# Optimization experiments

Measured on AMD Instinct MI355X. Metric: run time of the kernel, lower is better.

Reference implementation:

```python
import jax, jax.numpy as jnp
import numpy as np

B, SIZE_IN, SIZE_OUT = 64, 1024, 1024


def setup_inputs() -> dict:
    key = jax.random.key(0)
    ks = jax.random.split(key, 6)
    mu_in = jax.random.normal(ks[0], (B, SIZE_IN), jnp.float32)
    # PSD input covariance: low-rank + jitter (sigma_in is a covariance matrix)
    L = jax.random.normal(ks[1], (B, SIZE_IN, 16), jnp.float32)
    sigma_in = jnp.einsum('bik,bjk->bij', L, L) / 16.0 + 1e-3 * jnp.eye(SIZE_IN, dtype=jnp.float32)
    bound = (1.0 / SIZE_IN) ** 0.5
    w_mu = jax.random.uniform(ks[2], (SIZE_IN, SIZE_OUT), jnp.float32, -bound, bound)
    b_mu = jax.random.uniform(ks[3], (SIZE_OUT, 1), jnp.float32, -bound, bound)
    w_sigma = jax.random.uniform(ks[4], (SIZE_OUT, SIZE_IN), jnp.float32, -12.0, -2.0)
    b_sigma = jax.random.uniform(ks[5], (SIZE_OUT,), jnp.float32, -12.0, -2.0)
    return {"mu_in": mu_in, "sigma_in": sigma_in, "w_mu": w_mu,
            "w_sigma": w_sigma, "b_mu": b_mu, "b_sigma": b_sigma}


def reference(mu_in, sigma_in, w_mu, w_sigma, b_mu, b_sigma):
    Bsz, n = mu_in.shape            # n = size_in
    m = w_mu.shape[1]               # m = size_out
    # mean propagation: (B, m, 1)
    mu_out = jnp.einsum('io,bi->bo', w_mu, mu_in)[:, :, None] + b_mu
    # diagonal weight/bias variances (softplus + epsilon), kept as vectors
    W_Sig = jax.nn.softplus(w_sigma) + 1e-6   # (m, n) == diag of diag_embed(W_Sigma)[o]
    B_Sig = jax.nn.softplus(b_sigma) + 1e-6   # (m,)
    # mu_in^T diag(W_Sig[o]) mu_in  -> (B, m)
    quad = jnp.einsum('oi,bi->bo', W_Sig, mu_in * mu_in)
    # faithful replication of torch's .view-based "trace" term:
    # W_Sigma.view(m, n*n) @ sigma_in.view(n*n, B), then result.view(B, m).
    # diag_embed rows only hit flat indices i*(n+1), so gather those rows.
    sig_flat = sigma_in.reshape(n * n, Bsz)            # memory reinterpret, like torch .view
    diag_rows = sig_flat[jnp.arange(n) * (n + 1)]      # (n, B)
    trW = (W_Sig @ diag_rows).reshape(Bsz, m)          # memory reinterpret, like torch .view
    # w_mu^T sigma_in w_mu : (B, m, m) -- dominant GEMM
    muT_sig_mu = jnp.einsum('io,bij,jp->bop', w_mu, sigma_in, w_mu)
    diag_term = trW + quad + B_Sig[None, :]            # (B, m)
    Sigma_out = muT_sig_mu + diag_term[:, :, None] * jnp.eye(m, dtype=mu_in.dtype)
    # KL vs standard normal; slogdet of a positive diagonal matrix == sum(log(diag))
    w_kl = 0.5 * jnp.sum(jnp.sum(W_Sig, axis=1) + jnp.sum(w_mu * w_mu, axis=0)
                         - n - jnp.sum(jnp.log(W_Sig), axis=1))
    b_kl = 0.5 * (jnp.sum(B_Sig) + jnp.sum(b_mu * b_mu) - m - jnp.sum(jnp.log(B_Sig)))
    return (mu_out, Sigma_out, w_kl, b_kl)
```

## Files before the change

### kernel.cpp

```cpp
#include <hip/hip_runtime.h>
#include <hip/hip_bf16.h>


typedef short bf16x8 __attribute__((ext_vector_type(8)));
typedef float f32x4  __attribute__((ext_vector_type(4)));
typedef unsigned short u16x8 __attribute__((ext_vector_type(8)));

__device__ __forceinline__ unsigned short f2bf(float f) {
    union { float f; unsigned u; } a; a.f = f;
    unsigned u = a.u;
    u += 0x7fffu + ((u >> 16) & 1u);
    return (unsigned short)(u >> 16);
}

__device__ __forceinline__ float softplus_eps(float x) {
    return fmaxf(x, 0.f) + log1pf(expf(-fabsf(x))) + 1e-6f;
}

__device__ __forceinline__ void gload_lds16(const unsigned short* g, unsigned short* l) {
    __builtin_amdgcn_global_load_lds(
        (const __attribute__((address_space(1))) void*)g,
        (__attribute__((address_space(3))) void*)l, 16, 0, 0);
}


__global__ void k_zero(float* acc) {
    if (threadIdx.x < 16) acc[threadIdx.x] = 0.f;
}

__global__ void k_convert(const float* __restrict__ src, unsigned short* __restrict__ dst) {
    const size_t i = ((size_t)blockIdx.x * 256 + threadIdx.x) * 8;
    const float4 a = *(const float4*)(src + i);
    const float4 b = *(const float4*)(src + i + 4);
    u16x8 h;
    h[0] = f2bf(a.x); h[1] = f2bf(a.y); h[2] = f2bf(a.z); h[3] = f2bf(a.w);
    h[4] = f2bf(b.x); h[5] = f2bf(b.y); h[6] = f2bf(b.z); h[7] = f2bf(b.w);
    *(u16x8*)(dst + i) = h;
}

__global__ void k_transpose(const float* __restrict__ wmu, float* __restrict__ wT32,
                            unsigned short* __restrict__ wTb, float* __restrict__ acc) {
    __shared__ float tile[64][65];
    const int bx = blockIdx.x;
    const int by = blockIdx.y;
    const int t = threadIdx.x;
    const int r = t >> 4;
    const int c4 = (t & 15) * 4;
    float s = 0.f;
#pragma unroll
    for (int p = 0; p < 4; ++p) {
        const int row = r + p * 16;
        const float4 v = *(const float4*)(wmu + (size_t)(bx * 64 + row) * 1024 + by * 64 + c4);
        tile[row][c4 + 0] = v.x; tile[row][c4 + 1] = v.y;
        tile[row][c4 + 2] = v.z; tile[row][c4 + 3] = v.w;
        s += v.x * v.x + v.y * v.y + v.z * v.z + v.w * v.w;
    }
    __syncthreads();
#pragma unroll
    for (int p = 0; p < 4; ++p) {
        const int row = r + p * 16;
        float4 o;
        o.x = tile[c4 + 0][row]; o.y = tile[c4 + 1][row];
        o.z = tile[c4 + 2][row]; o.w = tile[c4 + 3][row];
        const size_t off = (size_t)(by * 64 + row) * 1024 + bx * 64 + c4;
        *(float4*)(wT32 + off) = o;
        ushort4 h; h.x = f2bf(o.x); h.y = f2bf(o.y); h.z = f2bf(o.z); h.w = f2bf(o.w);
        *(ushort4*)(wTb + off) = h;
    }
#pragma unroll
    for (int off = 32; off; off >>= 1) s += __shfl_down(s, off, 64);
    if ((t & 63) == 0) atomicAdd(acc + 1, s);
}

__global__ void k_wsig(const float* __restrict__ wsg, float* __restrict__ WSig,
                       float* __restrict__ acc) {
    const int idx = (blockIdx.x * 256 + threadIdx.x) * 4;
    const float4 x = *(const float4*)(wsg + idx);
    float4 w;
    w.x = softplus_eps(x.x); w.y = softplus_eps(x.y);
    w.z = softplus_eps(x.z); w.w = softplus_eps(x.w);
    *(float4*)(WSig + idx) = w;
    float sw = w.x + w.y + w.z + w.w;
    float sl = logf(w.x) + logf(w.y) + logf(w.z) + logf(w.w);
#pragma unroll
    for (int off = 32; off; off >>= 1) {
        sw += __shfl_down(sw, off, 64);
        sl += __shfl_down(sl, off, 64);
    }
    if ((threadIdx.x & 63) == 0) { atomicAdd(acc + 0, sw); atomicAdd(acc + 2, sl); }
}

__global__ void k_gather(const float* __restrict__ sig, float* __restrict__ dr) {
    const int tg = blockIdx.x * 256 + threadIdx.x;
    const int k = tg >> 6, q = tg & 63;
    dr[tg] = sig[(size_t)k * 65600 + q];
}

__global__ void k_small(const float* __restrict__ mu_in, const float* __restrict__ wT32,
                        const float* __restrict__ WSig, const float* __restrict__ dr,
                        const float* __restrict__ b_mu, const float* __restrict__ b_sig,
                        float* __restrict__ mu_out, float* __restrict__ dterm) {
    __shared__ float mu_s[1024];
    __shared__ float m2_s[1024];
    const int blk = blockIdx.x;
    const int b = blk >> 2;
    const int o0 = (blk & 3) * 256;
    const int t = threadIdx.x;
    const int o = o0 + t;
    for (int j = t; j < 1024; j += 256) {
        const float v = mu_in[b * 1024 + j];
        mu_s[j] = v; m2_s[j] = v * v;
    }
    __syncthreads();
    const int rowTr = b * 16 + (o >> 6);
    const int qq = o & 63;
    const float* wrow = wT32 + (size_t)o * 1024;
    const float* srow = WSig + (size_t)o * 1024;
    const float* trow = WSig + (size_t)rowTr * 1024;
    float am = 0.f, aq = 0.f, at = 0.f;
#pragma unroll 4
    for (int i = 0; i < 1024; i += 4) {
        const float4 wv = *(const float4*)(wrow + i);
        const float4 sv = *(const float4*)(srow + i);
        const float4 tv = *(const float4*)(trow + i);
        const float4 mv = *(const float4*)(&mu_s[i]);
        const float4 m2 = *(const float4*)(&m2_s[i]);
        am += wv.x * mv.x + wv.y * mv.y + wv.z * mv.z + wv.w * mv.w;
        aq += sv.x * m2.x + sv.y * m2.y + sv.z * m2.z + sv.w * m2.w;
        at += tv.x * dr[(i + 0) * 64 + qq] + tv.y * dr[(i + 1) * 64 + qq]
            + tv.z * dr[(i + 2) * 64 + qq] + tv.w * dr[(i + 3) * 64 + qq];
    }
    const float bs = softplus_eps(b_sig[o]);
    dterm[b * 1024 + o] = at + aq + bs;
    mu_out[b * 1024 + o] = am + b_mu[o];
}

__global__ void k_final(const float* __restrict__ b_mu, const float* __restrict__ b_sig,
                        const float* __restrict__ acc, float* __restrict__ out) {
    __shared__ float red[3][4];
    const int t = threadIdx.x, lane = t & 63, w = t >> 6;
    float s1 = 0.f, s2 = 0.f, s3 = 0.f;
    for (int i = t; i < 1024; i += 256) {
        const float sp = softplus_eps(b_sig[i]);
        s1 += sp; s2 += logf(sp);
        const float bm = b_mu[i]; s3 += bm * bm;
    }
#pragma unroll
    for (int off = 32; off; off >>= 1) {
        s1 += __shfl_down(s1, off, 64);
        s2 += __shfl_down(s2, off, 64);
        s3 += __shfl_down(s3, off, 64);
    }
    if (lane == 0) { red[0][w] = s1; red[1][w] = s2; red[2][w] = s3; }
    __syncthreads();
    if (t == 0) {
        const float S1 = red[0][0] + red[0][1] + red[0][2] + red[0][3];
        const float S2 = red[1][0] + red[1][1] + red[1][2] + red[1][3];
        const float S3 = red[2][0] + red[2][1] + red[2][2] + red[2][3];
        out[67174401] = 0.5f * (S1 + S3 - 1024.f - S2);
        out[67174400] = 0.5f * (acc[0] + acc[1] - 1048576.f - acc[2]);
    }
}

__global__ __launch_bounds__(256) void k_gemmA(const unsigned short* __restrict__ sigb,
                                               const unsigned short* __restrict__ wT,
                                               unsigned short* __restrict__ Tp) {
    __shared__ unsigned short As[128 * 64];
    __shared__ unsigned short Bs[128 * 64];
    const int it_ = blockIdx.x;
    const int pt_ = blockIdx.y;
    const int bz  = blockIdx.z;
    const int t = threadIdx.x;
    const int lane = t & 63, wave = t >> 6;
    const int wm = wave & 1, wn = wave >> 1;
    const int q = lane >> 4, r = lane & 15;
    const unsigned short* Ab = sigb + ((size_t)bz << 20) + (size_t)(it_ * 128) * 1024;
    const unsigned short* Bb = wT + (size_t)(pt_ * 128) * 1024;
    f32x4 acc[4][4];
#pragma unroll
    for (int a = 0; a < 4; ++a)
#pragma unroll
        for (int b2 = 0; b2 < 4; ++b2) acc[a][b2] = (f32x4){0.f, 0.f, 0.f, 0.f};
    const int srow = t >> 3;
    const int scol = (t & 7) * 8;
    for (int kt = 0; kt < 16; ++kt) {
        const int k0 = kt * 64;
        __syncthreads();
#pragma unroll
        for (int ps = 0; ps < 4; ++ps) {
            const int rr = ps * 32 + srow;
            gload_lds16(Ab + (size_t)rr * 1024 + k0 + scol, &As[ps * 2048 + t * 8]);
            gload_lds16(Bb + (size_t)rr * 1024 + k0 + scol, &Bs[ps * 2048 + t * 8]);
        }
        __syncthreads();
#pragma unroll
        for (int ks = 0; ks < 2; ++ks) {
            const int ko = ks * 32 + q * 8;
            bf16x8 af[4], bf[4];
#pragma unroll
            for (int tm = 0; tm < 4; ++tm)
                af[tm] = *(const bf16x8*)(&As[(wm * 64 + tm * 16 + r) * 64 + ko]);
#pragma unroll
            for (int tn = 0; tn < 4; ++tn)
                bf[tn] = *(const bf16x8*)(&Bs[(wn * 64 + tn * 16 + r) * 64 + ko]);
#pragma unroll
            for (int tm = 0; tm < 4; ++tm)
#pragma unroll
                for (int tn = 0; tn < 4; ++tn)
                    acc[tm][tn] = __builtin_amdgcn_mfma_f32_16x16x32_bf16(
                        af[tm], bf[tn], acc[tm][tn], 0, 0, 0);
        }
    }
    unsigned short* Tb = Tp + ((size_t)bz << 20);
#pragma unroll
    for (int tm = 0; tm < 4; ++tm)
#pragma unroll
        for (int tn = 0; tn < 4; ++tn) {
            const f32x4 v = acc[tm][tn];
            const int i_e = it_ * 128 + wm * 64 + tm * 16 + q * 4;
            const int p_e = pt_ * 128 + wn * 64 + tn * 16 + r;
            ushort4 h; h.x = f2bf(v[0]); h.y = f2bf(v[1]); h.z = f2bf(v[2]); h.w = f2bf(v[3]);
            *(ushort4*)(Tb + (size_t)p_e * 1024 + i_e) = h;
        }
}

__global__ __launch_bounds__(256) void k_gemmB(const unsigned short* __restrict__ wT,
                                               const unsigned short* __restrict__ Tp,
                                               const float* __restrict__ dterm,
                                               float* __restrict__ Cs) {
    __shared__ unsigned short As[128 * 64];
    __shared__ unsigned short Bs[128 * 64];
    int ot_ = 0, rem = blockIdx.x;
    while (rem >= 8 - ot_) { rem -= 8 - ot_; ++ot_; }
    const int pt_ = ot_ + rem;
    const int bz  = blockIdx.z;
    const int t = threadIdx.x;
    const int lane = t & 63, wave = t >> 6;
    const int wm = wave & 1, wn = wave >> 1;
    const int q = lane >> 4, r = lane & 15;
    const unsigned short* Ab = wT + (size_t)(ot_ * 128) * 1024;
    const unsigned short* Bb = Tp + ((size_t)bz << 20) + (size_t)(pt_ * 128) * 1024;
    f32x4 acc[4][4];
#pragma unroll
    for (int a = 0; a < 4; ++a)
#pragma unroll
        for (int b2 = 0; b2 < 4; ++b2) acc[a][b2] = (f32x4){0.f, 0.f, 0.f, 0.f};
    const int srow = t >> 3;
    const int scol = (t & 7) * 8;
    for (int kt = 0; kt < 16; ++kt) {
        const int k0 = kt * 64;
        __syncthreads();
#pragma unroll
        for (int ps = 0; ps < 4; ++ps) {
            const int rr = ps * 32 + srow;
            gload_lds16(Ab + (size_t)rr * 1024 + k0 + scol, &As[ps * 2048 + t * 8]);
            gload_lds16(Bb + (size_t)rr * 1024 + k0 + scol, &Bs[ps * 2048 + t * 8]);
        }
        __syncthreads();
#pragma unroll
        for (int ks = 0; ks < 2; ++ks) {
            const int ko = ks * 32 + q * 8;
            bf16x8 af[4], bf[4];
#pragma unroll
            for (int tm = 0; tm < 4; ++tm)
                af[tm] = *(const bf16x8*)(&As[(wm * 64 + tm * 16 + r) * 64 + ko]);
#pragma unroll
            for (int tn = 0; tn < 4; ++tn)
                bf[tn] = *(const bf16x8*)(&Bs[(wn * 64 + tn * 16 + r) * 64 + ko]);
#pragma unroll
            for (int tm = 0; tm < 4; ++tm)
#pragma unroll
                for (int tn = 0; tn < 4; ++tn)
                    acc[tm][tn] = __builtin_amdgcn_mfma_f32_16x16x32_bf16(
                        af[tm], bf[tn], acc[tm][tn], 0, 0, 0);
        }
    }
    float* Cb = Cs + ((size_t)bz << 20);
    if (ot_ == pt_) {
#pragma unroll
        for (int tm = 0; tm < 4; ++tm)
#pragma unroll
            for (int tn = 0; tn < 4; ++tn) {
                const f32x4 v = acc[tm][tn];
                const int o_b = ot_ * 128 + wm * 64 + tm * 16 + q * 4;
                const int p_e = pt_ * 128 + wn * 64 + tn * 16 + r;
#pragma unroll
                for (int j = 0; j < 4; ++j) {
                    const int o = o_b + j;
                    float x = v[j];
                    if (o == p_e) x += dterm[bz * 1024 + o];
                    Cb[(size_t)o * 1024 + p_e] = x;
                }
            }
    } else {
#pragma unroll
        for (int tm = 0; tm < 4; ++tm)
#pragma unroll
            for (int tn = 0; tn < 4; ++tn) {
                const f32x4 v = acc[tm][tn];
                const int o_b = ot_ * 128 + wm * 64 + tm * 16 + q * 4;
                const int p_e = pt_ * 128 + wn * 64 + tn * 16 + r;
#pragma unroll
                for (int j = 0; j < 4; ++j)
                    Cb[(size_t)(o_b + j) * 1024 + p_e] = v[j];
                *(float4*)(Cb + (size_t)p_e * 1024 + o_b) =
                    (float4){v[0], v[1], v[2], v[3]};
            }
    }
}


extern "C" void kernel_launch(void* const* d_in, const int* in_sizes, int n_in,
                              void* d_out, int out_size, void* d_ws, size_t ws_size,
                              hipStream_t stream) {
    (void)in_sizes; (void)n_in; (void)out_size; (void)ws_size;
    const float* mu_in = (const float*)d_in[0];
    const float* sigma = (const float*)d_in[1];
    const float* w_mu  = (const float*)d_in[2];
    const float* w_sig = (const float*)d_in[3];
    const float* b_mu  = (const float*)d_in[4];
    const float* b_sg  = (const float*)d_in[5];
    float* out = (float*)d_out;

    char* ws = (char*)d_ws;
    unsigned short* Tp   = (unsigned short*)(ws + 0x0);
    float*          wT32 = (float*)(ws + 0x8000000);
    float*          WSig = (float*)(ws + 0x8400000);
    unsigned short* wTb  = (unsigned short*)(ws + 0x8800000);
    float*          dr   = (float*)(ws + 0x8A00000);
    float*          dt   = (float*)(ws + 0x8A40000);
    float*          acc  = (float*)(ws + 0x8A80000);

    unsigned short* sigb = (unsigned short*)(out + 65536);

    k_zero<<<1, 64, 0, stream>>>(acc);
    k_convert<<<32768, 256, 0, stream>>>(sigma, sigb);
    k_transpose<<<dim3(16, 16), 256, 0, stream>>>(w_mu, wT32, wTb, acc);
    k_wsig<<<1024, 256, 0, stream>>>(w_sig, WSig, acc);
    k_gather<<<256, 256, 0, stream>>>(sigma, dr);
    k_small<<<256, 256, 0, stream>>>(mu_in, wT32, WSig, dr, b_mu, b_sg, out, dt);
    k_final<<<1, 256, 0, stream>>>(b_mu, b_sg, acc, out);
    k_gemmA<<<dim3(8, 8, 64), 256, 0, stream>>>(sigb, wTb, Tp);
    k_gemmB<<<dim3(36, 1, 64), 256, 0, stream>>>(wTb, Tp, dt, out + 65536);
}
```

Baseline: 1.020 ms.

## Enlarge GEMM tiles to 256x256 with double-buffered swizzled LDS pipeline

Both batched GEMMs now use 256x256 output tiles computed by 512-thread blocks, with 8x4 MFMA accumulators per wave. The K loop double-buffers 128 KB of dynamic LDS, prefetching two stages ahead and waiting on partial vmcnt counts instead of syncing on every load. LDS columns are XOR-swizzled to avoid bank conflicts, and s_setprio raises priority around the MFMA bursts. The aim is more data reuse per tile and overlap of global loads with compute. The cost is higher register pressure and occupancy of about one block per CU, and the symmetric gemmB grid shrinks to 10 tiles per batch.

```diff
diff --git a/kernel.cpp b/kernel.cpp
--- a/kernel.cpp
+++ b/kernel.cpp
@@ -162,128 +162,134 @@
     }
 }
 
-__global__ __launch_bounds__(256) void k_gemmA(const unsigned short* __restrict__ sigb,
+
+__device__ __forceinline__ void stage_tile(const unsigned short* __restrict__ gsrc,
+                                           unsigned short* ldst, int t, int k0) {
+    const int tr = t >> 3;
+    const int swz = (((t & 7) ^ (tr & 7)) << 3);
+#pragma unroll
+    for (int pass = 0; pass < 4; ++pass) {
+        const int row = pass * 64 + tr;
+        gload_lds16(gsrc + (size_t)row * 1024 + k0 + swz, ldst + pass * 4096 + t * 8);
+    }
+}
+
+__device__ __forceinline__ void compute_tile(const unsigned short* Al, const unsigned short* Bl,
+                                             f32x4 (&acc)[8][4], int wm, int wn, int q, int r) {
+    const int swz = (r & 7) << 3;
+#pragma unroll
+    for (int ks = 0; ks < 2; ++ks) {
+        const int co = (ks * 32 + q * 8) ^ swz;
+        bf16x8 af[8], bv[4];
+#pragma unroll
+        for (int tm = 0; tm < 8; ++tm)
+            af[tm] = *(const bf16x8*)(&Al[(wm * 128 + tm * 16 + r) * 64 + co]);
+#pragma unroll
+        for (int tn = 0; tn < 4; ++tn)
+            bv[tn] = *(const bf16x8*)(&Bl[(wn * 64 + tn * 16 + r) * 64 + co]);
+        __builtin_amdgcn_s_setprio(1);
+#pragma unroll
+        for (int tm = 0; tm < 8; ++tm)
+#pragma unroll
+            for (int tn = 0; tn < 4; ++tn)
+                acc[tm][tn] = __builtin_amdgcn_mfma_f32_16x16x32_bf16(
+                    af[tm], bv[tn], acc[tm][tn], 0, 0, 0);
+        __builtin_amdgcn_s_setprio(0);
+    }
+}
+
+__device__ __forceinline__ void run_gemm(const unsigned short* __restrict__ Ab,
+                                         const unsigned short* __restrict__ Bb,
+                                         unsigned short* lds, f32x4 (&acc)[8][4], int t) {
+    const int lane = t & 63;
+    const int wid = t >> 6;
+    const int wm = wid >> 2, wn = wid & 3;
+    const int q = lane >> 4, r = lane & 15;
+#pragma unroll
+    for (int a = 0; a < 8; ++a)
+#pragma unroll
+        for (int b = 0; b < 4; ++b) acc[a][b] = (f32x4){0.f, 0.f, 0.f, 0.f};
+
+    stage_tile(Ab, lds + 0,     t, 0);
+    stage_tile(Bb, lds + 16384, t, 0);
+    stage_tile(Ab, lds + 32768, t, 64);
+    stage_tile(Bb, lds + 49152, t, 64);
+    asm volatile("s_waitcnt vmcnt(8)" ::: "memory");
+    asm volatile("s_barrier" ::: "memory");
+
+    for (int kt = 0; kt < 16; ++kt) {
+        unsigned short* buf = lds + (kt & 1) * 32768;
+        compute_tile(buf, buf + 16384, acc, wm, wn, q, r);
+        asm volatile("s_waitcnt lgkmcnt(0)" ::: "memory");
+        __builtin_amdgcn_sched_barrier(0);
+        asm volatile("s_barrier" ::: "memory");
+        if (kt + 2 < 16) {
+            stage_tile(Ab, buf, t, (kt + 2) * 64);
+            stage_tile(Bb, buf + 16384, t, (kt + 2) * 64);
+            asm volatile("s_waitcnt vmcnt(8)" ::: "memory");
+        } else {
+            asm volatile("s_waitcnt vmcnt(0)" ::: "memory");
+        }
+        asm volatile("s_barrier" ::: "memory");
+    }
+}
+
+__global__ __launch_bounds__(512) void k_gemmA(const unsigned short* __restrict__ sigb,
                                                const unsigned short* __restrict__ wT,
                                                unsigned short* __restrict__ Tp) {
-    __shared__ unsigned short As[128 * 64];
-    __shared__ unsigned short Bs[128 * 64];
+    extern __shared__ unsigned short lds[];
     const int it_ = blockIdx.x;
     const int pt_ = blockIdx.y;
     const int bz  = blockIdx.z;
     const int t = threadIdx.x;
-    const int lane = t & 63, wave = t >> 6;
-    const int wm = wave & 1, wn = wave >> 1;
+    const unsigned short* Ab = sigb + ((size_t)bz << 20) + (size_t)(it_ * 256) * 1024;
+    const unsigned short* Bb = wT + (size_t)(pt_ * 256) * 1024;
+    f32x4 acc[8][4];
+    run_gemm(Ab, Bb, lds, acc, t);
+
+    const int lane = t & 63, wid = t >> 6;
+    const int wm = wid >> 2, wn = wid & 3;
     const int q = lane >> 4, r = lane & 15;
-    const unsigned short* Ab = sigb + ((size_t)bz << 20) + (size_t)(it_ * 128) * 1024;
-    const unsigned short* Bb = wT + (size_t)(pt_ * 128) * 1024;
-    f32x4 acc[4][4];
-#pragma unroll
-    for (int a = 0; a < 4; ++a)
-#pragma unroll
-        for (int b2 = 0; b2 < 4; ++b2) acc[a][b2] = (f32x4){0.f, 0.f, 0.f, 0.f};
-    const int srow = t >> 3;
-    const int scol = (t & 7) * 8;
-    for (int kt = 0; kt < 16; ++kt) {
-        const int k0 = kt * 64;
-        __syncthreads();
-#pragma unroll
-        for (int ps = 0; ps < 4; ++ps) {
-            const int rr = ps * 32 + srow;
-            gload_lds16(Ab + (size_t)rr * 1024 + k0 + scol, &As[ps * 2048 + t * 8]);
-            gload_lds16(Bb + (size_t)rr * 1024 + k0 + scol, &Bs[ps * 2048 + t * 8]);
-        }
-        __syncthreads();
-#pragma unroll
-        for (int ks = 0; ks < 2; ++ks) {
-            const int ko = ks * 32 + q * 8;
-            bf16x8 af[4], bf[4];
-#pragma unroll
-            for (int tm = 0; tm < 4; ++tm)
-                af[tm] = *(const bf16x8*)(&As[(wm * 64 + tm * 16 + r) * 64 + ko]);
-#pragma unroll
-            for (int tn = 0; tn < 4; ++tn)
-                bf[tn] = *(const bf16x8*)(&Bs[(wn * 64 + tn * 16 + r) * 64 + ko]);
-#pragma unroll
-            for (int tm = 0; tm < 4; ++tm)
-#pragma unroll
-                for (int tn = 0; tn < 4; ++tn)
-                    acc[tm][tn] = __builtin_amdgcn_mfma_f32_16x16x32_bf16(
-                        af[tm], bf[tn], acc[tm][tn], 0, 0, 0);
-        }
-    }
     unsigned short* Tb = Tp + ((size_t)bz << 20);
 #pragma unroll
-    for (int tm = 0; tm < 4; ++tm)
+    for (int tm = 0; tm < 8; ++tm)
 #pragma unroll
         for (int tn = 0; tn < 4; ++tn) {
             const f32x4 v = acc[tm][tn];
-            const int i_e = it_ * 128 + wm * 64 + tm * 16 + q * 4;
-            const int p_e = pt_ * 128 + wn * 64 + tn * 16 + r;
+            const int i_e = it_ * 256 + wm * 128 + tm * 16 + q * 4;
+            const int p_e = pt_ * 256 + wn * 64 + tn * 16 + r;
             ushort4 h; h.x = f2bf(v[0]); h.y = f2bf(v[1]); h.z = f2bf(v[2]); h.w = f2bf(v[3]);
             *(ushort4*)(Tb + (size_t)p_e * 1024 + i_e) = h;
         }
 }
 
-__global__ __launch_bounds__(256) void k_gemmB(const unsigned short* __restrict__ wT,
+__global__ __launch_bounds__(512) void k_gemmB(const unsigned short* __restrict__ wT,
                                                const unsigned short* __restrict__ Tp,
                                                const float* __restrict__ dterm,
                                                float* __restrict__ Cs) {
-    __shared__ unsigned short As[128 * 64];
-    __shared__ unsigned short Bs[128 * 64];
+    extern __shared__ unsigned short lds[];
     int ot_ = 0, rem = blockIdx.x;
-    while (rem >= 8 - ot_) { rem -= 8 - ot_; ++ot_; }
+    while (rem >= 4 - ot_) { rem -= 4 - ot_; ++ot_; }
     const int pt_ = ot_ + rem;
     const int bz  = blockIdx.z;
     const int t = threadIdx.x;
-    const int lane = t & 63, wave = t >> 6;
-    const int wm = wave & 1, wn = wave >> 1;
+    const unsigned short* Ab = wT + (size_t)(ot_ * 256) * 1024;
+    const unsigned short* Bb = Tp + ((size_t)bz << 20) + (size_t)(pt_ * 256) * 1024;
+    f32x4 acc[8][4];
+    run_gemm(Ab, Bb, lds, acc, t);
+
+    const int lane = t & 63, wid = t >> 6;
+    const int wm = wid >> 2, wn = wid & 3;
     const int q = lane >> 4, r = lane & 15;
-    const unsigned short* Ab = wT + (size_t)(ot_ * 128) * 1024;
-    const unsigned short* Bb = Tp + ((size_t)bz << 20) + (size_t)(pt_ * 128) * 1024;
-    f32x4 acc[4][4];
-#pragma unroll
-    for (int a = 0; a < 4; ++a)
-#pragma unroll
-        for (int b2 = 0; b2 < 4; ++b2) acc[a][b2] = (f32x4){0.f, 0.f, 0.f, 0.f};
-    const int srow = t >> 3;
-    const int scol = (t & 7) * 8;
-    for (int kt = 0; kt < 16; ++kt) {
-        const int k0 = kt * 64;
-        __syncthreads();
-#pragma unroll
-        for (int ps = 0; ps < 4; ++ps) {
-            const int rr = ps * 32 + srow;
-            gload_lds16(Ab + (size_t)rr * 1024 + k0 + scol, &As[ps * 2048 + t * 8]);
-            gload_lds16(Bb + (size_t)rr * 1024 + k0 + scol, &Bs[ps * 2048 + t * 8]);
-        }
-        __syncthreads();
-#pragma unroll
-        for (int ks = 0; ks < 2; ++ks) {
-            const int ko = ks * 32 + q * 8;
-            bf16x8 af[4], bf[4];
-#pragma unroll
-            for (int tm = 0; tm < 4; ++tm)
-                af[tm] = *(const bf16x8*)(&As[(wm * 64 + tm * 16 + r) * 64 + ko]);
-#pragma unroll
-            for (int tn = 0; tn < 4; ++tn)
-                bf[tn] = *(const bf16x8*)(&Bs[(wn * 64 + tn * 16 + r) * 64 + ko]);
-#pragma unroll
-            for (int tm = 0; tm < 4; ++tm)
-#pragma unroll
-                for (int tn = 0; tn < 4; ++tn)
-                    acc[tm][tn] = __builtin_amdgcn_mfma_f32_16x16x32_bf16(
-                        af[tm], bf[tn], acc[tm][tn], 0, 0, 0);
-        }
-    }
     float* Cb = Cs + ((size_t)bz << 20);
     if (ot_ == pt_) {
 #pragma unroll
-        for (int tm = 0; tm < 4; ++tm)
+        for (int tm = 0; tm < 8; ++tm)
 #pragma unroll
             for (int tn = 0; tn < 4; ++tn) {
                 const f32x4 v = acc[tm][tn];
-                const int o_b = ot_ * 128 + wm * 64 + tm * 16 + q * 4;
-                const int p_e = pt_ * 128 + wn * 64 + tn * 16 + r;
+                const int o_b = ot_ * 256 + wm * 128 + tm * 16 + q * 4;
+                const int p_e = pt_ * 256 + wn * 64 + tn * 16 + r;
 #pragma unroll
                 for (int j = 0; j < 4; ++j) {
                     const int o = o_b + j;
@@ -294,12 +300,12 @@
             }
     } else {
 #pragma unroll
-        for (int tm = 0; tm < 4; ++tm)
+        for (int tm = 0; tm < 8; ++tm)
 #pragma unroll
             for (int tn = 0; tn < 4; ++tn) {
                 const f32x4 v = acc[tm][tn];
-                const int o_b = ot_ * 128 + wm * 64 + tm * 16 + q * 4;
-                const int p_e = pt_ * 128 + wn * 64 + tn * 16 + r;
+                const int o_b = ot_ * 256 + wm * 128 + tm * 16 + q * 4;
+                const int p_e = pt_ * 256 + wn * 64 + tn * 16 + r;
 #pragma unroll
                 for (int j = 0; j < 4; ++j)
                     Cb[(size_t)(o_b + j) * 1024 + p_e] = v[j];
@@ -333,6 +339,15 @@
 
     unsigned short* sigb = (unsigned short*)(out + 65536);
 
+    static bool attr_set = false;
+    if (!attr_set) {
+        hipFuncSetAttribute((const void*)k_gemmA,
+                            hipFuncAttributeMaxDynamicSharedMemorySize, 131072);
+        hipFuncSetAttribute((const void*)k_gemmB,
+                            hipFuncAttributeMaxDynamicSharedMemorySize, 131072);
+        attr_set = true;
+    }
+
     k_zero<<<1, 64, 0, stream>>>(acc);
     k_convert<<<32768, 256, 0, stream>>>(sigma, sigb);
     k_transpose<<<dim3(16, 16), 256, 0, stream>>>(w_mu, wT32, wTb, acc);
@@ -340,6 +355,6 @@
     k_gather<<<256, 256, 0, stream>>>(sigma, dr);
     k_small<<<256, 256, 0, stream>>>(mu_in, wT32, WSig, dr, b_mu, b_sg, out, dt);
     k_final<<<1, 256, 0, stream>>>(b_mu, b_sg, acc, out);
-    k_gemmA<<<dim3(8, 8, 64), 256, 0, stream>>>(sigb, wTb, Tp);
-    k_gemmB<<<dim3(36, 1, 64), 256, 0, stream>>>(wTb, Tp, dt, out + 65536);
-}
+    k_gemmA<<<dim3(4, 4, 64), 512, 131072, stream>>>(sigb, wTb, Tp);
+    k_gemmB<<<dim3(10, 1, 64), 512, 131072, stream>>>(wTb, Tp, dt, out + 65536);
+}
```

Result: faster. 968.1 us (-5.1%).
